# Performance work log

Measured on AMD Instinct MI355X. Metric: run time of the kernel, lower is better.

## Reference

```python
import jax, jax.numpy as jnp
import numpy as np

TOPK = 100
SCALE = 4.0

def setup_inputs() -> dict:
    key = jax.random.key(0)
    k1, k2, k3 = jax.random.split(key, 3)
    B, C, H, W = 16, 80, 256, 256
    x = jax.random.normal(k1, (B, C, H, W), dtype=jnp.float32)
    wh = jax.random.uniform(k2, (B, 2, H, W), dtype=jnp.float32)
    reg = jax.random.normal(k3, (B, 2, H, W), dtype=jnp.float32)
    return {"x": x, "wh": wh, "reg": reg}

def reference(x, wh, reg):
    B, C, H, W = x.shape
    # top-k over flattened class*spatial scores
    scores, indices = jax.lax.top_k(x.reshape(B, -1), TOPK)  # [B, K]
    # torch int/int is true division -> float (faithful to source)
    topk_classes = indices / (H * W)                  # [B, K] float
    topk_indices = indices % (W * W)                  # [B, K] int (source uses out_w**2; H==W)
    topk_ys = topk_indices / W                        # float
    topk_xs = topk_indices % W                        # int
    # [B, H*W, 2] channel-last views
    center = reg.transpose(0, 2, 3, 1).reshape(B, -1, 2)
    whp = wh.transpose(0, 2, 3, 1).reshape(B, -1, 2)
    # gather per-detection offsets / sizes
    xs_off = jnp.take_along_axis(center[..., 0], topk_indices, axis=1)  # [B, K]
    ys_off = jnp.take_along_axis(center[..., 1], topk_indices, axis=1)
    w = jnp.take_along_axis(whp[..., 0], topk_indices, axis=1)
    h = jnp.take_along_axis(whp[..., 1], topk_indices, axis=1)
    cx = topk_xs + xs_off
    cy = topk_ys + ys_off
    half_w = w / 2
    half_h = h / 2
    results = jnp.stack([cx - half_w, cy - half_h, cx + half_w, cy + half_h], axis=-1)
    return (topk_classes, scores, results * SCALE)
```

## Files before the change

### kernel.cpp

```cpp
#include <hip/hip_runtime.h>
#include <stdint.h>
#include <limits.h>

#define Bn      16
#define Nn      5242880
#define KK      100
#define BPB     128
#define CHUNK   (Nn / BPB)
#define SLOT    24
#define SORTCAP 2048
#define RANKCAP 256
#define NBINS   4096
#define T0      4.0f
#define FTH     256

typedef float f4v __attribute__((ext_vector_type(4)));

__device__ __forceinline__ unsigned fkey(unsigned u) {
    return (u & 0x80000000u) ? ~u : (u | 0x80000000u);
}

__global__ __launch_bounds__(256) void k_collect(const float* __restrict__ x,
                                                 int* __restrict__ bcnt,
                                                 float* __restrict__ cval,
                                                 int* __restrict__ cidx) {
    const int b = blockIdx.y, blk = blockIdx.x;
    __shared__ int lcnt;
    if (threadIdx.x == 0) lcnt = 0;
    __syncthreads();
    const f4v* xv = reinterpret_cast<const f4v*>(
        x + (size_t)b * Nn + (size_t)blk * CHUNK);
    const int base = blk * CHUNK;
    float* v  = cval + ((size_t)b * BPB + blk) * SLOT;
    int*   ix = cidx + ((size_t)b * BPB + blk) * SLOT;
#pragma unroll 4
    for (int j = threadIdx.x; j < CHUNK / 4; j += 256) {
        f4v f = __builtin_nontemporal_load(&xv[j]);
        const float m = fmaxf(fmaxf(f.x, f.y), fmaxf(f.z, f.w));
        if (m >= T0) {
            const int i0 = base + 4 * j;
            if (f.x >= T0) { int p = atomicAdd(&lcnt, 1); if (p < SLOT) { v[p] = f.x; ix[p] = i0;     } }
            if (f.y >= T0) { int p = atomicAdd(&lcnt, 1); if (p < SLOT) { v[p] = f.y; ix[p] = i0 + 1; } }
            if (f.z >= T0) { int p = atomicAdd(&lcnt, 1); if (p < SLOT) { v[p] = f.z; ix[p] = i0 + 2; } }
            if (f.w >= T0) { int p = atomicAdd(&lcnt, 1); if (p < SLOT) { v[p] = f.w; ix[p] = i0 + 3; } }
        }
    }
    __syncthreads();
    if (threadIdx.x == 0) bcnt[b * BPB + blk] = lcnt;
}

__device__ __forceinline__ void emit_one(int b, int rank, float val, int idx,
                                         const float* __restrict__ wh,
                                         const float* __restrict__ reg,
                                         float* __restrict__ out) {
    float* out_cls = out;
    float* out_scr = out + Bn * KK;
    float* out_res = out + 2 * Bn * KK;
    out_cls[b * KK + rank] = (float)idx * (1.0f / 65536.0f);
    out_scr[b * KK + rank] = val;
    const int s  = idx & 65535;
    const float tys = (float)s * (1.0f / 256.0f);
    const float txs = (float)(s & 255);
    const float xo = reg[(size_t)(b * 2 + 0) * 65536 + s];
    const float yo = reg[(size_t)(b * 2 + 1) * 65536 + s];
    const float ww = wh [(size_t)(b * 2 + 0) * 65536 + s];
    const float hh = wh [(size_t)(b * 2 + 1) * 65536 + s];
    const float cx = txs + xo;
    const float cy = tys + yo;
    const float hw  = ww * 0.5f;
    const float hh2 = hh * 0.5f;
    float* r = out_res + (size_t)(b * KK + rank) * 4;
    r[0] = (cx - hw)  * 4.0f;
    r[1] = (cy - hh2) * 4.0f;
    r[2] = (cx + hw)  * 4.0f;
    r[3] = (cy + hh2) * 4.0f;
}

__global__ __launch_bounds__(FTH) void k_final(const float* __restrict__ x,
                                               const float* __restrict__ wh,
                                               const float* __restrict__ reg,
                                               const int* __restrict__ bcnt,
                                               const float* __restrict__ cval,
                                               const int* __restrict__ cidx,
                                               float* __restrict__ out) {
    const int b = blockIdx.x;
    const int t = threadIdx.x;
    __shared__ float sv[SORTCAP];
    __shared__ int   si[SORTCAP];
    __shared__ int   scan[BPB];
    __shared__ int   hist[NBINS];
    __shared__ int   sflags;
    __shared__ int   scnt;
    __shared__ unsigned stk;

    if (t == 0) { sflags = 0; scnt = 0; }
    __syncthreads();

    int c = 0;
    if (t < BPB) {
        c = bcnt[b * BPB + t];
        if (c > SLOT) atomicOr(&sflags, 1);
        scan[t] = c;
    }
    __syncthreads();
    for (int off = 1; off < BPB; off <<= 1) {
        int vv = 0;
        if (t < BPB) { vv = scan[t]; if (t >= off) vv += scan[t - off]; }
        __syncthreads();
        if (t < BPB) scan[t] = vv;
        __syncthreads();
    }
    const int total_all = scan[BPB - 1];
    const bool bad = (sflags != 0) || (total_all < KK) || (total_all > SORTCAP);

    const float NEG_INF = __int_as_float(0xFF800000);
    int n;
    if (!bad) {
        n = total_all;
        for (int i = t; i < SORTCAP; i += FTH) { sv[i] = NEG_INF; si[i] = INT_MAX; }
        __syncthreads();
        if (t < BPB) {
            const int off = scan[t] - c;
            const float* v  = cval + ((size_t)b * BPB + t) * SLOT;
            const int*   ix = cidx + ((size_t)b * BPB + t) * SLOT;
            for (int i = 0; i < c; ++i) { sv[off + i] = v[i]; si[off + i] = ix[i]; }
        }
        __syncthreads();
    } else {
        for (int i = t; i < NBINS; i += FTH) hist[i] = 0;
        for (int i = t; i < SORTCAP; i += FTH) { sv[i] = NEG_INF; si[i] = INT_MAX; }
        __syncthreads();
        const float4* xv = reinterpret_cast<const float4*>(x + (size_t)b * Nn);
        for (int j = t; j < Nn / 4; j += FTH) {
            float4 f = xv[j];
            atomicAdd(&hist[fkey(__float_as_uint(f.x)) >> 20], 1);
            atomicAdd(&hist[fkey(__float_as_uint(f.y)) >> 20], 1);
            atomicAdd(&hist[fkey(__float_as_uint(f.z)) >> 20], 1);
            atomicAdd(&hist[fkey(__float_as_uint(f.w)) >> 20], 1);
        }
        __syncthreads();
        if (t == 0) {
            int cum = 0; unsigned k = 0;
            for (int bin = NBINS - 1; bin >= 0; --bin) {
                cum += hist[bin];
                if (cum >= KK) { k = (unsigned)bin << 20; break; }
            }
            stk = k;
        }
        __syncthreads();
        const unsigned tk = stk;
        for (int j = t; j < Nn / 4; j += FTH) {
            float4 f = xv[j];
            const int i0 = 4 * j;
            float a[4] = {f.x, f.y, f.z, f.w};
#pragma unroll
            for (int cc = 0; cc < 4; ++cc) {
                if (fkey(__float_as_uint(a[cc])) >= tk) {
                    int p = atomicAdd(&scnt, 1);
                    if (p < SORTCAP) { sv[p] = a[cc]; si[p] = i0 + cc; }
                }
            }
        }
        __syncthreads();
        n = scnt; if (n > SORTCAP) n = SORTCAP;
    }

    if (!bad && n <= RANKCAP) {
        const float myv = sv[t];
        const int   myi = si[t];
        int rank = 0;
#pragma unroll 8
        for (int j = 0; j < RANKCAP; ++j) {
            const float vj = sv[j];
            const int   ij = si[j];
            rank += ((vj > myv) || (vj == myv && ij < myi)) ? 1 : 0;
        }
        if (rank < KK) emit_one(b, rank, myv, myi, wh, reg, out);
        return;
    }

    int pad = FTH;
    while (pad < n) pad <<= 1;
    for (int k = 2; k <= pad; k <<= 1) {
        for (int j = k >> 1; j > 0; j >>= 1) {
            for (int i = t; i < pad; i += FTH) {
                const int ixj = i ^ j;
                if (ixj > i) {
                    float va = sv[i], vb = sv[ixj];
                    int   ia = si[i], ib = si[ixj];
                    const bool a_before_b = (va > vb) || (va == vb && ia < ib);
                    const bool dir = ((i & k) == 0);
                    if (dir ? !a_before_b : a_before_b) {
                        sv[i] = vb; sv[ixj] = va; si[i] = ib; si[ixj] = ia;
                    }
                }
            }
            __syncthreads();
        }
    }
    for (int j = t; j < KK; j += FTH) emit_one(b, j, sv[j], si[j], wh, reg, out);
}

extern "C" void kernel_launch(void* const* d_in, const int* in_sizes, int n_in,
                              void* d_out, int out_size, void* d_ws, size_t ws_size,
                              hipStream_t stream) {
    const float* x   = (const float*)d_in[0];
    const float* wh  = (const float*)d_in[1];
    const float* reg = (const float*)d_in[2];
    float* out = (float*)d_out;

    char* ws = (char*)d_ws;
    int*   bcnt = (int*)(ws);
    float* cval = (float*)(ws + 16 * 1024);
    int*   cidx = (int*)(ws + 16 * 1024 + (size_t)Bn * BPB * SLOT * 4);

    dim3 gridS(BPB, Bn);
    k_collect<<<gridS, 256, 0, stream>>>(x, bcnt, cval, cidx);
    k_final  <<<Bn,    FTH, 0, stream>>>(x, wh, reg, bcnt, cval, cidx, out);
}
```

Baseline: 63.59 us.

## Fuse collect and final kernels using last-block-done atomic counter per batch

Merges the per-chunk threshold collection and the per-batch final selection into one kernel. The last block of each batch is detected with an atomic counter and performs the merge, rank and emit. Shared memory is reduced by aliasing the histogram with the sort buffers. This removes a kernel launch boundary and the idle tail of a 16-block second kernel, at the cost of a memset launch and serialized final work inside the last block.

```diff
diff --git a/kernel.cpp b/kernel.cpp
--- a/kernel.cpp
+++ b/kernel.cpp
@@ -18,35 +18,6 @@
 
 __device__ __forceinline__ unsigned fkey(unsigned u) {
     return (u & 0x80000000u) ? ~u : (u | 0x80000000u);
-}
-
-__global__ __launch_bounds__(256) void k_collect(const float* __restrict__ x,
-                                                 int* __restrict__ bcnt,
-                                                 float* __restrict__ cval,
-                                                 int* __restrict__ cidx) {
-    const int b = blockIdx.y, blk = blockIdx.x;
-    __shared__ int lcnt;
-    if (threadIdx.x == 0) lcnt = 0;
-    __syncthreads();
-    const f4v* xv = reinterpret_cast<const f4v*>(
-        x + (size_t)b * Nn + (size_t)blk * CHUNK);
-    const int base = blk * CHUNK;
-    float* v  = cval + ((size_t)b * BPB + blk) * SLOT;
-    int*   ix = cidx + ((size_t)b * BPB + blk) * SLOT;
-#pragma unroll 4
-    for (int j = threadIdx.x; j < CHUNK / 4; j += 256) {
-        f4v f = __builtin_nontemporal_load(&xv[j]);
-        const float m = fmaxf(fmaxf(f.x, f.y), fmaxf(f.z, f.w));
-        if (m >= T0) {
-            const int i0 = base + 4 * j;
-            if (f.x >= T0) { int p = atomicAdd(&lcnt, 1); if (p < SLOT) { v[p] = f.x; ix[p] = i0;     } }
-            if (f.y >= T0) { int p = atomicAdd(&lcnt, 1); if (p < SLOT) { v[p] = f.y; ix[p] = i0 + 1; } }
-            if (f.z >= T0) { int p = atomicAdd(&lcnt, 1); if (p < SLOT) { v[p] = f.z; ix[p] = i0 + 2; } }
-            if (f.w >= T0) { int p = atomicAdd(&lcnt, 1); if (p < SLOT) { v[p] = f.w; ix[p] = i0 + 3; } }
-        }
-    }
-    __syncthreads();
-    if (threadIdx.x == 0) bcnt[b * BPB + blk] = lcnt;
 }
 
 __device__ __forceinline__ void emit_one(int b, int rank, float val, int idx,
@@ -76,22 +47,60 @@
     r[3] = (cy + hh2) * 4.0f;
 }
 
-__global__ __launch_bounds__(FTH) void k_final(const float* __restrict__ x,
-                                               const float* __restrict__ wh,
-                                               const float* __restrict__ reg,
-                                               const int* __restrict__ bcnt,
-                                               const float* __restrict__ cval,
-                                               const int* __restrict__ cidx,
-                                               float* __restrict__ out) {
-    const int b = blockIdx.x;
+__global__ __launch_bounds__(FTH, 8) void k_fused(const float* __restrict__ x,
+                                                  const float* __restrict__ wh,
+                                                  const float* __restrict__ reg,
+                                                  int* __restrict__ done,
+                                                  int* __restrict__ bcnt,
+                                                  float* __restrict__ cval,
+                                                  int* __restrict__ cidx,
+                                                  float* __restrict__ out) {
+    const int b = blockIdx.y, blk = blockIdx.x;
     const int t = threadIdx.x;
-    __shared__ float sv[SORTCAP];
-    __shared__ int   si[SORTCAP];
-    __shared__ int   scan[BPB];
-    __shared__ int   hist[NBINS];
-    __shared__ int   sflags;
-    __shared__ int   scnt;
+
+    __shared__ int lcnt;
+    __shared__ int amlast;
+    __shared__ int uw[2 * SORTCAP];
+    __shared__ int scan[BPB];
+    __shared__ int sflags;
+    __shared__ int scnt;
     __shared__ unsigned stk;
+
+    if (t == 0) lcnt = 0;
+    __syncthreads();
+    {
+        const f4v* xv = reinterpret_cast<const f4v*>(
+            x + (size_t)b * Nn + (size_t)blk * CHUNK);
+        const int base = blk * CHUNK;
+        float* v  = cval + ((size_t)b * BPB + blk) * SLOT;
+        int*   ix = cidx + ((size_t)b * BPB + blk) * SLOT;
+#pragma unroll 4
+        for (int j = t; j < CHUNK / 4; j += FTH) {
+            f4v f = __builtin_nontemporal_load(&xv[j]);
+            const float m = fmaxf(fmaxf(f.x, f.y), fmaxf(f.z, f.w));
+            if (m >= T0) {
+                const int i0 = base + 4 * j;
+                if (f.x >= T0) { int p = atomicAdd(&lcnt, 1); if (p < SLOT) { v[p] = f.x; ix[p] = i0;     } }
+                if (f.y >= T0) { int p = atomicAdd(&lcnt, 1); if (p < SLOT) { v[p] = f.y; ix[p] = i0 + 1; } }
+                if (f.z >= T0) { int p = atomicAdd(&lcnt, 1); if (p < SLOT) { v[p] = f.z; ix[p] = i0 + 2; } }
+                if (f.w >= T0) { int p = atomicAdd(&lcnt, 1); if (p < SLOT) { v[p] = f.w; ix[p] = i0 + 3; } }
+            }
+        }
+    }
+    __syncthreads();
+    if (t == 0) {
+        bcnt[b * BPB + blk] = lcnt;
+        __threadfence();
+        amlast = (atomicAdd(&done[b], 1) == BPB - 1) ? 1 : 0;
+    }
+    __syncthreads();
+    if (!amlast) return;
+
+    __threadfence();
+
+    float* sv   = (float*)uw;
+    int*   si   = uw + SORTCAP;
+    int*   hist = uw;
 
     if (t == 0) { sflags = 0; scnt = 0; }
     __syncthreads();
@@ -128,11 +137,10 @@
         __syncthreads();
     } else {
         for (int i = t; i < NBINS; i += FTH) hist[i] = 0;
-        for (int i = t; i < SORTCAP; i += FTH) { sv[i] = NEG_INF; si[i] = INT_MAX; }
-        __syncthreads();
-        const float4* xv = reinterpret_cast<const float4*>(x + (size_t)b * Nn);
+        __syncthreads();
+        const float4* xv4 = reinterpret_cast<const float4*>(x + (size_t)b * Nn);
         for (int j = t; j < Nn / 4; j += FTH) {
-            float4 f = xv[j];
+            float4 f = xv4[j];
             atomicAdd(&hist[fkey(__float_as_uint(f.x)) >> 20], 1);
             atomicAdd(&hist[fkey(__float_as_uint(f.y)) >> 20], 1);
             atomicAdd(&hist[fkey(__float_as_uint(f.z)) >> 20], 1);
@@ -140,17 +148,19 @@
         }
         __syncthreads();
         if (t == 0) {
-            int cum = 0; unsigned k = 0;
+            int cum = 0; unsigned k2 = 0;
             for (int bin = NBINS - 1; bin >= 0; --bin) {
                 cum += hist[bin];
-                if (cum >= KK) { k = (unsigned)bin << 20; break; }
-            }
-            stk = k;
+                if (cum >= KK) { k2 = (unsigned)bin << 20; break; }
+            }
+            stk = k2;
         }
         __syncthreads();
         const unsigned tk = stk;
+        for (int i = t; i < SORTCAP; i += FTH) { sv[i] = NEG_INF; si[i] = INT_MAX; }
+        __syncthreads();
         for (int j = t; j < Nn / 4; j += FTH) {
-            float4 f = xv[j];
+            float4 f = xv4[j];
             const int i0 = 4 * j;
             float a[4] = {f.x, f.y, f.z, f.w};
 #pragma unroll
@@ -211,10 +221,12 @@
 
     char* ws = (char*)d_ws;
     int*   bcnt = (int*)(ws);
+    int*   done = (int*)(ws + 8 * 1024);
     float* cval = (float*)(ws + 16 * 1024);
     int*   cidx = (int*)(ws + 16 * 1024 + (size_t)Bn * BPB * SLOT * 4);
 
-    dim3 gridS(BPB, Bn);
-    k_collect<<<gridS, 256, 0, stream>>>(x, bcnt, cval, cidx);
-    k_final  <<<Bn,    FTH, 0, stream>>>(x, wh, reg, bcnt, cval, cidx, out);
-}
+    hipMemsetAsync(done, 0, Bn * sizeof(int), stream);
+
+    dim3 grid(BPB, Bn);
+    k_fused<<<grid, FTH, 0, stream>>>(x, wh, reg, done, bcnt, cval, cidx, out);
+}
```

Measured after the change: 154.9 us. +143.6%, slower.
